# Kernel optimization log

Measured on AMD Instinct MI355X. Metric: run time of the kernel, lower is better.

The kernel has to match this reference:

```python
import jax, jax.numpy as jnp
import numpy as np

D_MODEL = 1024
N_HEADS = 16
HEAD_DIM = D_MODEL // N_HEADS
NEG_INF = -1e10


def setup_inputs() -> dict:
    key = jax.random.key(0)
    ks = jax.random.split(key, 6)
    B, S = 2, 2048
    x = jax.random.normal(ks[0], (B, S, D_MODEL), dtype=jnp.float32)
    mask = jnp.ones((B, S), dtype=jnp.int32)
    scale_w = 1.0 / np.sqrt(D_MODEL)
    Wq = jax.random.normal(ks[1], (D_MODEL, D_MODEL), dtype=jnp.float32) * scale_w
    Wk = jax.random.normal(ks[2], (D_MODEL, D_MODEL), dtype=jnp.float32) * scale_w
    Wv = jax.random.normal(ks[3], (D_MODEL, D_MODEL), dtype=jnp.float32) * scale_w
    Wo = jax.random.normal(ks[4], (D_MODEL, D_MODEL), dtype=jnp.float32) * scale_w
    bq = jnp.zeros((D_MODEL,), jnp.float32)
    bk = jnp.zeros((D_MODEL,), jnp.float32)
    bv = jnp.zeros((D_MODEL,), jnp.float32)
    bo = jnp.zeros((D_MODEL,), jnp.float32)
    return {"x": x, "mask": mask, "Wq": Wq, "bq": bq, "Wk": Wk, "bk": bk,
            "Wv": Wv, "bv": bv, "Wo": Wo, "bo": bo}


def reference(x, mask, Wq, bq, Wk, bk, Wv, bv, Wo, bo):
    B, S, _ = x.shape
    # Linear projections (torch Linear: y = x @ W.T + b)
    Q = x @ Wq.T + bq
    K = x @ Wk.T + bk
    V = x @ Wv.T + bv
    # [B, H, S, Dh]
    Q = Q.reshape(B, S, N_HEADS, HEAD_DIM).transpose(0, 2, 1, 3)
    K = K.reshape(B, S, N_HEADS, HEAD_DIM).transpose(0, 2, 1, 3)
    V = V.reshape(B, S, N_HEADS, HEAD_DIM).transpose(0, 2, 1, 3)
    scale = jnp.sqrt(jnp.float32(HEAD_DIM))
    energy = jnp.einsum('bhqd,bhkd->bhqk', Q, K) / scale  # [B,H,S,S]
    # mask: [B,S] -> broadcast over heads and query dim (keys masked)
    m = mask[:, None, None, :]  # [B,1,1,S]
    energy = jnp.where(m == 0, jnp.float32(NEG_INF), energy)
    attention = jax.nn.softmax(energy, axis=-1)
    # dropout in eval mode = identity
    out = jnp.einsum('bhqk,bhkd->bhqd', attention, V)  # [B,H,S,Dh]
    out = out.transpose(0, 2, 1, 3).reshape(B, S, D_MODEL)
    return out @ Wo.T + bo
```

## Files before the change

### kernel.cpp

```cpp
#include <hip/hip_runtime.h>
#include <hip/hip_bf16.h>

typedef __hip_bfloat16 bf16;
typedef __attribute__((ext_vector_type(8))) short s8v;
typedef __attribute__((ext_vector_type(4))) float f4v;

#define D_MODEL 1024
#define S_LEN   2048
#define BATCH   2
#define NH      16
#define HD      64
#define M_TOTAL 4096
#define NT      (S_LEN / 64)

__device__ __forceinline__ void gll16(const bf16* g, bf16* l) {
    __builtin_amdgcn_global_load_lds(
        (const __attribute__((address_space(1))) void*)g,
        (__attribute__((address_space(3))) void*)l, 16, 0, 0);
}

__global__ __launch_bounds__(256) void cvt_bf16x8(const float* __restrict__ s,
                                                  bf16* __restrict__ d, int n) {
    int i = (blockIdx.x * 256 + threadIdx.x) * 8;
    if (i < n) {
        float4 a = *(const float4*)(s + i);
        float4 b = *(const float4*)(s + i + 4);
        union { bf16 h[8]; uint4 u; } p;
        p.h[0] = __float2bfloat16(a.x); p.h[1] = __float2bfloat16(a.y);
        p.h[2] = __float2bfloat16(a.z); p.h[3] = __float2bfloat16(a.w);
        p.h[4] = __float2bfloat16(b.x); p.h[5] = __float2bfloat16(b.y);
        p.h[6] = __float2bfloat16(b.z); p.h[7] = __float2bfloat16(b.w);
        *(uint4*)(d + i) = p.u;
    }
}

struct WPtrs { const float* s0; const float* s1; const float* s2; const float* s3;
               bf16* d0; bf16* d1; bf16* d2; bf16* d3; };

__global__ __launch_bounds__(256) void cvt_w(WPtrs p) {
    const float* s; bf16* d;
    switch (blockIdx.y) {
        case 0:  s = p.s0; d = p.d0; break;
        case 1:  s = p.s1; d = p.d1; break;
        case 2:  s = p.s2; d = p.d2; break;
        default: s = p.s3; d = p.d3; break;
    }
    int i = (blockIdx.x * 256 + threadIdx.x) * 8;
    float4 a = *(const float4*)(s + i);
    float4 b = *(const float4*)(s + i + 4);
    union { bf16 h[8]; uint4 u; } q;
    q.h[0] = __float2bfloat16(a.x); q.h[1] = __float2bfloat16(a.y);
    q.h[2] = __float2bfloat16(a.z); q.h[3] = __float2bfloat16(a.w);
    q.h[4] = __float2bfloat16(b.x); q.h[5] = __float2bfloat16(b.y);
    q.h[6] = __float2bfloat16(b.z); q.h[7] = __float2bfloat16(b.w);
    *(uint4*)(d + i) = q.u;
}

template<int TM, int TN>
__device__ __forceinline__ void gemm_main(const bf16* __restrict__ A,
                                          const bf16* __restrict__ W,
                                          bf16* As, bf16* Bs,
                                          int bm, int bn,
                                          f4v (&acc)[TM/32][TN/32])
{
    constexpr int FM = TM / 32, FN = TN / 32;
    constexpr int CALLS_A = TM / 16, CALLS = (TM + TN) / 16, PW = CALLS / 4;
    const int t = threadIdx.x, wv = t >> 6, lane = t & 63;
    const int quad = lane >> 4, l15 = lane & 15;
    const int wm = (wv >> 1) * (TM / 2), wn = (wv & 1) * (TN / 2);
    const int lr = lane >> 2, lc = (lane & 3) * 8;

    auto STAGE = [&](int buf, int k0) {
        #pragma unroll
        for (int c = 0; c < PW; ++c) {
            const int cc = wv * PW + c;
            if (cc < CALLS_A) {
                gll16(A + (size_t)(bm + cc * 16 + lr) * D_MODEL + k0 + lc,
                      As + buf * (TM * 32) + cc * 16 * 32);
            } else {
                const int r2 = cc - CALLS_A;
                gll16(W + (size_t)(bn + r2 * 16 + lr) * D_MODEL + k0 + lc,
                      Bs + buf * (TN * 32) + r2 * 16 * 32);
            }
        }
    };

    STAGE(0, 0);
    __syncthreads();
    int cur = 0;

    for (int k0 = 0; k0 < D_MODEL; k0 += 32) {
        if (k0 + 32 < D_MODEL) STAGE(cur ^ 1, k0 + 32);

        const bf16* ab = As + cur * (TM * 32);
        const bf16* bb = Bs + cur * (TN * 32);
        s8v af[FM], bfv[FN];
        #pragma unroll
        for (int i = 0; i < FM; ++i)
            af[i] = *(const s8v*)(ab + (wm + i * 16 + l15) * 32 + quad * 8);
        #pragma unroll
        for (int j = 0; j < FN; ++j)
            bfv[j] = *(const s8v*)(bb + (wn + j * 16 + l15) * 32 + quad * 8);
        __builtin_amdgcn_s_setprio(1);
        #pragma unroll
        for (int i = 0; i < FM; ++i)
            #pragma unroll
            for (int j = 0; j < FN; ++j)
                acc[i][j] = __builtin_amdgcn_mfma_f32_16x16x32_bf16(af[i], bfv[j], acc[i][j], 0, 0, 0);
        __builtin_amdgcn_s_setprio(0);

        __syncthreads();
        cur ^= 1;
    }
}

__global__ __launch_bounds__(256) void gemm_qkv(
    const bf16* __restrict__ x,
    const bf16* __restrict__ Wq, const bf16* __restrict__ Wk, const bf16* __restrict__ Wv,
    const float* __restrict__ bq, const float* __restrict__ bk, const float* __restrict__ bv,
    bf16* __restrict__ Qb, bf16* __restrict__ Kb, bf16* __restrict__ Vtb)
{
    __shared__ __align__(16) char smem[4 * 64 * 72 * 2];
    bf16* As = (bf16*)smem;
    bf16* Bs = (bf16*)(smem + 2 * 128 * 32 * 2);
    bf16 (*Tw)[64][72] = (bf16(*)[64][72])smem;

    const int z = blockIdx.z;
    const bf16*  W    = (z == 0) ? Wq : (z == 1) ? Wk : Wv;
    const float* bias = (z == 0) ? bq : (z == 1) ? bk : bv;
    bf16*        out  = (z == 0) ? Qb : (z == 1) ? Kb : Vtb;
    const int bm = blockIdx.y * 128, bn = blockIdx.x * 128;

    f4v acc[4][4] = {};
    gemm_main<128, 128>(x, W, As, Bs, bm, bn, acc);

    const int t = threadIdx.x, wv = t >> 6, lane = t & 63;
    const int quad = lane >> 4, l15 = lane & 15;
    const int wm = (wv >> 1) * 64, wn = (wv & 1) * 64;

    if (z == 2) {
        __syncthreads();
        #pragma unroll
        for (int j = 0; j < 4; ++j) {
            const int col = bn + wn + j * 16 + l15;
            const float bv_ = bias[col];
            #pragma unroll
            for (int i = 0; i < 4; ++i) {
                #pragma unroll
                for (int rp = 0; rp < 4; rp += 2) {
                    union { bf16 h[2]; unsigned u; } p2;
                    p2.h[0] = __float2bfloat16(acc[i][j][rp]     + bv_);
                    p2.h[1] = __float2bfloat16(acc[i][j][rp + 1] + bv_);
                    *(unsigned*)&Tw[wv][j * 16 + l15][i * 16 + quad * 4 + rp] = p2.u;
                }
            }
        }
        const int bb = (bm + wm) >> 11, s0 = (bm + wm) & 2047;
        #pragma unroll
        for (int p = 0; p < 8; ++p) {
            const int dl = p * 8 + (lane >> 3);
            const int sl = (lane & 7) * 8;
            const int col = bn + wn + dl;
            const int h = col >> 6, d = col & 63;
            uint4 v = *(const uint4*)&Tw[wv][dl][sl];
            *(uint4*)&out[(((size_t)(bb * NH + h)) * HD + d) * S_LEN + s0 + sl] = v;
        }
    } else {
        #pragma unroll
        for (int j = 0; j < 4; ++j) {
            const int col = bn + wn + j * 16 + l15;
            const float bv_ = bias[col];
            const int h = col >> 6, d = col & 63;
            #pragma unroll
            for (int i = 0; i < 4; ++i) {
                #pragma unroll
                for (int r = 0; r < 4; ++r) {
                    const int row = bm + wm + i * 16 + quad * 4 + r;
                    const int b = row >> 11, s = row & 2047;
                    const float v = acc[i][j][r] + bv_;
                    out[(((size_t)(b * NH + h)) * S_LEN + s) * HD + d] = __float2bfloat16(v);
                }
            }
        }
    }
}

__global__ __launch_bounds__(256) void gemm_out(
    const bf16* __restrict__ Ob, const bf16* __restrict__ Wo,
    const float* __restrict__ bo, float* __restrict__ out)
{
    __shared__ __align__(16) bf16 As[2][64 * 32];
    __shared__ __align__(16) bf16 Bs[2][128 * 32];
    const int bm = blockIdx.y * 64, bn = blockIdx.x * 128;

    f4v acc[2][4] = {};
    gemm_main<64, 128>(Ob, Wo, &As[0][0], &Bs[0][0], bm, bn, acc);

    const int t = threadIdx.x, wv = t >> 6, lane = t & 63;
    const int quad = lane >> 4, l15 = lane & 15;
    const int wm = (wv >> 1) * 32, wn = (wv & 1) * 64;
    #pragma unroll
    for (int j = 0; j < 4; ++j) {
        const int col = bn + wn + j * 16 + l15;
        const float bv_ = bo[col];
        #pragma unroll
        for (int i = 0; i < 2; ++i)
            #pragma unroll
            for (int r = 0; r < 4; ++r) {
                const int row = bm + wm + i * 16 + quad * 4 + r;
                out[(size_t)row * D_MODEL + col] = acc[i][j][r] + bv_;
            }
    }
}

__global__ __launch_bounds__(256) void attn_mfma(
    const bf16* __restrict__ Q, const bf16* __restrict__ K,
    const bf16* __restrict__ Vt, const int* __restrict__ mask,
    bf16* __restrict__ O)
{
    __shared__ __align__(16) bf16 Ks[64][64];
    __shared__ __align__(16) bf16 Vts[64][64];
    __shared__ __align__(16) bf16 Ps[4][16][64];
    __shared__ float mb[64];

    const int t = threadIdx.x, wv = t >> 6, lane = t & 63;
    const int quad = lane >> 4, l15 = lane & 15;
    const int sw = l15 & 7;
    const int bid = blockIdx.x;
    const int b = bid & 1, h = (bid >> 1) & 15, qt = bid >> 5;
    const int q0 = qt * 64;
    const size_t qkbase = ((size_t)(b * NH + h)) * S_LEN * HD;
    const size_t vtbase = ((size_t)(b * NH + h)) * HD * S_LEN;

    const float KSC  = 0.125f * 1.44269504f;
    const float THR2 = 8.0f * 1.44269504f;

    const bf16* qrow = Q + qkbase + (size_t)(q0 + wv * 16 + l15) * HD;
    const s8v qf0 = *(const s8v*)(qrow + quad * 8);
    const s8v qf1 = *(const s8v*)(qrow + 32 + quad * 8);

    const int srow = t >> 2;
    const int swr  = srow & 7;
    const int c2   = (t & 3) * 2;
    const int ch0  = c2 ^ swr, ch1 = (c2 + 1) ^ swr;

    uint4 kr0, kr1, vr0, vr1; int mr = 1;
    auto LOADT = [&](int kt2) {
        const int kk = kt2 * 64;
        const uint4* kp = (const uint4*)(K  + qkbase + (size_t)(kk + srow) * HD + c2 * 8);
        const uint4* vp = (const uint4*)(Vt + vtbase + (size_t)srow * S_LEN + kk + c2 * 8);
        kr0 = kp[0]; kr1 = kp[1];
        vr0 = vp[0]; vr1 = vp[1];
        if (t < 64) mr = mask[b * S_LEN + kk + t];
    };
    auto STAGE = [&]() {
        *(uint4*)&Ks[srow][ch0 * 8]  = kr0;
        *(uint4*)&Ks[srow][ch1 * 8]  = kr1;
        *(uint4*)&Vts[srow][ch0 * 8] = vr0;
        *(uint4*)&Vts[srow][ch1 * 8] = vr1;
        if (t < 64) mb[t] = mr ? 0.f : -1e30f;
    };

    LOADT(0);

    float mprev = -1e30f, lsum = 0.f;
    f4v oacc[4] = {};

    for (int kt = 0; kt < NT; ++kt) {
        __syncthreads();
        STAGE();
        __syncthreads();
        if (kt + 1 < NT) LOADT(kt + 1);

        f4v st[4];
        __builtin_amdgcn_s_setprio(1);
        #pragma unroll
        for (int c = 0; c < 4; ++c) {
            const char* kr = (const char*)&Ks[c * 16 + l15][0];
            s8v kf0 = *(const s8v*)(kr + ((quad ^ sw) << 4));
            s8v kf1 = *(const s8v*)(kr + (((4 + quad) ^ sw) << 4));
            f4v z = {0.f, 0.f, 0.f, 0.f};
            z = __builtin_amdgcn_mfma_f32_16x16x32_bf16(kf0, qf0, z, 0, 0, 0);
            z = __builtin_amdgcn_mfma_f32_16x16x32_bf16(kf1, qf1, z, 0, 0, 0);
            st[c] = z;
        }
        __builtin_amdgcn_s_setprio(0);

        float mt = -1e30f;
        #pragma unroll
        for (int c = 0; c < 4; ++c) {
            const f4v m4 = *(const f4v*)&mb[c * 16 + quad * 4];
            st[c] = st[c] * KSC + m4;
            mt = fmaxf(mt, fmaxf(fmaxf(st[c][0], st[c][1]), fmaxf(st[c][2], st[c][3])));
        }
        mt = fmaxf(mt, __shfl_xor(mt, 16, 64));
        mt = fmaxf(mt, __shfl_xor(mt, 32, 64));

        float mn = mprev;
        if (!__all(mt <= mprev + THR2)) {
            mn = fmaxf(mprev, mt);
            const float alpha = __builtin_amdgcn_exp2f(mprev - mn);
            mprev = mn;
            float av[4];
            #pragma unroll
            for (int r = 0; r < 4; ++r) av[r] = __shfl(alpha, quad * 4 + r, 64);
            #pragma unroll
            for (int dt = 0; dt < 4; ++dt)
                #pragma unroll
                for (int r = 0; r < 4; ++r) oacc[dt][r] *= av[r];
            lsum *= alpha;
        }

        f4v psv = {0.f, 0.f, 0.f, 0.f};
        #pragma unroll
        for (int c = 0; c < 4; ++c) {
            f4v e = st[c] - mn;
            e[0] = __builtin_amdgcn_exp2f(e[0]);
            e[1] = __builtin_amdgcn_exp2f(e[1]);
            e[2] = __builtin_amdgcn_exp2f(e[2]);
            e[3] = __builtin_amdgcn_exp2f(e[3]);
            st[c] = e;
            psv += e;
        }
        lsum += psv[0] + psv[1] + psv[2] + psv[3];

        char* pr = (char*)&Ps[wv][l15][0];
        #pragma unroll
        for (int c = 0; c < 4; ++c) {
            union { bf16 hh[4]; short4 s4; } pk;
            pk.hh[0] = __float2bfloat16(st[c][0]);
            pk.hh[1] = __float2bfloat16(st[c][1]);
            pk.hh[2] = __float2bfloat16(st[c][2]);
            pk.hh[3] = __float2bfloat16(st[c][3]);
            const int wch = (2 * c + (quad >> 1)) ^ sw;
            *(short4*)(pr + (wch << 4) + ((quad & 1) << 3)) = pk.s4;
        }
        s8v pf0 = *(const s8v*)(pr + ((quad ^ sw) << 4));
        s8v pf1 = *(const s8v*)(pr + (((4 + quad) ^ sw) << 4));

        __builtin_amdgcn_s_setprio(1);
        #pragma unroll
        for (int dt = 0; dt < 4; ++dt) {
            const char* vr = (const char*)&Vts[dt * 16 + l15][0];
            s8v vf0 = *(const s8v*)(vr + ((quad ^ sw) << 4));
            s8v vf1 = *(const s8v*)(vr + (((4 + quad) ^ sw) << 4));
            oacc[dt] = __builtin_amdgcn_mfma_f32_16x16x32_bf16(pf0, vf0, oacc[dt], 0, 0, 0);
            oacc[dt] = __builtin_amdgcn_mfma_f32_16x16x32_bf16(pf1, vf1, oacc[dt], 0, 0, 0);
        }
        __builtin_amdgcn_s_setprio(0);
    }

    lsum += __shfl_xor(lsum, 16, 64);
    lsum += __shfl_xor(lsum, 32, 64);
    float linv[4];
    #pragma unroll
    for (int r = 0; r < 4; ++r) linv[r] = 1.f / __shfl(lsum, quad * 4 + r, 64);
    #pragma unroll
    for (int dt = 0; dt < 4; ++dt) {
        #pragma unroll
        for (int r = 0; r < 4; ++r) {
            const int s = q0 + wv * 16 + quad * 4 + r;
            const int col = h * 64 + dt * 16 + l15;
            O[((size_t)b * S_LEN + s) * D_MODEL + col] = __float2bfloat16(oacc[dt][r] * linv[r]);
        }
    }
}

extern "C" void kernel_launch(void* const* d_in, const int* in_sizes, int n_in,
                              void* d_out, int out_size, void* d_ws, size_t ws_size,
                              hipStream_t stream) {
    const float* x    = (const float*)d_in[0];
    const int*   mask = (const int*)  d_in[1];
    const float* Wq   = (const float*)d_in[2];
    const float* bq   = (const float*)d_in[3];
    const float* Wk   = (const float*)d_in[4];
    const float* bk   = (const float*)d_in[5];
    const float* Wv   = (const float*)d_in[6];
    const float* bv   = (const float*)d_in[7];
    const float* Wo   = (const float*)d_in[8];
    const float* bo   = (const float*)d_in[9];
    float* out = (float*)d_out;

    char* w = (char*)d_ws;
    bf16* xb  = (bf16*)w; w += (size_t)M_TOTAL * D_MODEL * 2;
    bf16* Wqb = (bf16*)w; w += (size_t)D_MODEL * D_MODEL * 2;
    bf16* Wkb = (bf16*)w; w += (size_t)D_MODEL * D_MODEL * 2;
    bf16* Wvb = (bf16*)w; w += (size_t)D_MODEL * D_MODEL * 2;
    bf16* Wob = (bf16*)w; w += (size_t)D_MODEL * D_MODEL * 2;
    bf16* Qb  = (bf16*)w; w += (size_t)M_TOTAL * D_MODEL * 2;
    bf16* Kb  = (bf16*)w; w += (size_t)M_TOTAL * D_MODEL * 2;
    bf16* Vtb = (bf16*)w; w += (size_t)M_TOTAL * D_MODEL * 2;
    bf16* Ob  = (bf16*)w; w += (size_t)M_TOTAL * D_MODEL * 2;

    const int nx = M_TOTAL * D_MODEL;
    cvt_bf16x8<<<nx / 2048, 256, 0, stream>>>(x, xb, nx);
    WPtrs wp = { Wq, Wk, Wv, Wo, Wqb, Wkb, Wvb, Wob };
    cvt_w<<<dim3(D_MODEL * D_MODEL / 2048, 4), 256, 0, stream>>>(wp);

    gemm_qkv<<<dim3(8, 32, 3), 256, 0, stream>>>(xb, Wqb, Wkb, Wvb, bq, bk, bv, Qb, Kb, Vtb);

    attn_mfma<<<BATCH * NH * (S_LEN / 64), 256, 0, stream>>>(Qb, Kb, Vtb, mask, Ob);

    gemm_out<<<dim3(8, 64), 256, 0, stream>>>(Ob, Wob, bo, out);
}
```

Baseline: 222.4 us.

## Double attention key tile to 128 and read mask directly from global

Result: slower. 372.6 us (+67.6%).

```diff
diff --git a/kernel.cpp b/kernel.cpp
--- a/kernel.cpp
+++ b/kernel.cpp
@@ -11,7 +11,6 @@
 #define NH      16
 #define HD      64
 #define M_TOTAL 4096
-#define NT      (S_LEN / 64)
 
 __device__ __forceinline__ void gll16(const bf16* g, bf16* l) {
     __builtin_amdgcn_global_load_lds(
@@ -218,16 +217,15 @@
     const bf16* __restrict__ Vt, const int* __restrict__ mask,
     bf16* __restrict__ O)
 {
-    __shared__ __align__(16) bf16 Ks[64][64];
-    __shared__ __align__(16) bf16 Vts[64][64];
+    __shared__ __align__(16) bf16 Ks[128][64];
+    __shared__ __align__(16) bf16 Vts[64][128];
     __shared__ __align__(16) bf16 Ps[4][16][64];
-    __shared__ float mb[64];
 
     const int t = threadIdx.x, wv = t >> 6, lane = t & 63;
     const int quad = lane >> 4, l15 = lane & 15;
     const int sw = l15 & 7;
     const int bid = blockIdx.x;
-    const int b = bid & 1, h = (bid >> 1) & 15, qt = bid >> 5;
+    const int qt = bid & 31, h = (bid >> 5) & 15, b = bid >> 9;
     const int q0 = qt * 64;
     const size_t qkbase = ((size_t)(b * NH + h)) * S_LEN * HD;
     const size_t vtbase = ((size_t)(b * NH + h)) * HD * S_LEN;
@@ -239,26 +237,26 @@
     const s8v qf0 = *(const s8v*)(qrow + quad * 8);
     const s8v qf1 = *(const s8v*)(qrow + 32 + quad * 8);
 
-    const int srow = t >> 2;
-    const int swr  = srow & 7;
-    const int c2   = (t & 3) * 2;
-    const int ch0  = c2 ^ swr, ch1 = (c2 + 1) ^ swr;
-
-    uint4 kr0, kr1, vr0, vr1; int mr = 1;
+    const int krow = t >> 1, kcb = (t & 1) * 4;
+    const int vrow = t >> 2, vcb = (t & 3) * 4;
+
+    uint4 kr[4], vr[4];
     auto LOADT = [&](int kt2) {
-        const int kk = kt2 * 64;
-        const uint4* kp = (const uint4*)(K  + qkbase + (size_t)(kk + srow) * HD + c2 * 8);
-        const uint4* vp = (const uint4*)(Vt + vtbase + (size_t)srow * S_LEN + kk + c2 * 8);
-        kr0 = kp[0]; kr1 = kp[1];
-        vr0 = vp[0]; vr1 = vp[1];
-        if (t < 64) mr = mask[b * S_LEN + kk + t];
+        const int kk = kt2 * 128;
+        const bf16* kp = K  + qkbase + (size_t)(kk + krow) * HD + kcb * 8;
+        const bf16* vp = Vt + vtbase + (size_t)vrow * S_LEN + kk + vcb * 8;
+        #pragma unroll
+        for (int j = 0; j < 4; ++j) kr[j] = *(const uint4*)(kp + j * 8);
+        #pragma unroll
+        for (int j = 0; j < 4; ++j) vr[j] = *(const uint4*)(vp + j * 8);
     };
     auto STAGE = [&]() {
-        *(uint4*)&Ks[srow][ch0 * 8]  = kr0;
-        *(uint4*)&Ks[srow][ch1 * 8]  = kr1;
-        *(uint4*)&Vts[srow][ch0 * 8] = vr0;
-        *(uint4*)&Vts[srow][ch1 * 8] = vr1;
-        if (t < 64) mb[t] = mr ? 0.f : -1e30f;
+        #pragma unroll
+        for (int j = 0; j < 4; ++j)
+            *(uint4*)&Ks[krow][((kcb + j) ^ (krow & 7)) * 8] = kr[j];
+        #pragma unroll
+        for (int j = 0; j < 4; ++j)
+            *(uint4*)&Vts[vrow][((vcb + j) ^ (vrow & 7)) * 8] = vr[j];
     };
 
     LOADT(0);
@@ -266,19 +264,21 @@
     float mprev = -1e30f, lsum = 0.f;
     f4v oacc[4] = {};
 
-    for (int kt = 0; kt < NT; ++kt) {
+    for (int kt = 0; kt < S_LEN / 128; ++kt) {
         __syncthreads();
         STAGE();
         __syncthreads();
-        if (kt + 1 < NT) LOADT(kt + 1);
-
-        f4v st[4];
+        if (kt + 1 < S_LEN / 128) LOADT(kt + 1);
+
+        const int kk = kt * 128;
+
+        f4v st[8];
         __builtin_amdgcn_s_setprio(1);
         #pragma unroll
-        for (int c = 0; c < 4; ++c) {
-            const char* kr = (const char*)&Ks[c * 16 + l15][0];
-            s8v kf0 = *(const s8v*)(kr + ((quad ^ sw) << 4));
-            s8v kf1 = *(const s8v*)(kr + (((4 + quad) ^ sw) << 4));
+        for (int c = 0; c < 8; ++c) {
+            const char* krd = (const char*)&Ks[c * 16 + l15][0];
+            s8v kf0 = *(const s8v*)(krd + ((quad ^ sw) << 4));
+            s8v kf1 = *(const s8v*)(krd + (((4 + quad) ^ sw) << 4));
             f4v z = {0.f, 0.f, 0.f, 0.f};
             z = __builtin_amdgcn_mfma_f32_16x16x32_bf16(kf0, qf0, z, 0, 0, 0);
             z = __builtin_amdgcn_mfma_f32_16x16x32_bf16(kf1, qf1, z, 0, 0, 0);
@@ -288,8 +288,13 @@
 
         float mt = -1e30f;
         #pragma unroll
-        for (int c = 0; c < 4; ++c) {
-            const f4v m4 = *(const f4v*)&mb[c * 16 + quad * 4];
+        for (int c = 0; c < 8; ++c) {
+            const int4 mkc = *(const int4*)&mask[b * S_LEN + kk + c * 16 + quad * 4];
+            f4v m4;
+            m4[0] = mkc.x ? 0.f : -1e30f;
+            m4[1] = mkc.y ? 0.f : -1e30f;
+            m4[2] = mkc.z ? 0.f : -1e30f;
+            m4[3] = mkc.w ? 0.f : -1e30f;
             st[c] = st[c] * KSC + m4;
             mt = fmaxf(mt, fmaxf(fmaxf(st[c][0], st[c][1]), fmaxf(st[c][2], st[c][3])));
         }
@@ -313,7 +318,7 @@
 
         f4v psv = {0.f, 0.f, 0.f, 0.f};
         #pragma unroll
-        for (int c = 0; c < 4; ++c) {
+        for (int c = 0; c < 8; ++c) {
             f4v e = st[c] - mn;
             e[0] = __builtin_amdgcn_exp2f(e[0]);
             e[1] = __builtin_amdgcn_exp2f(e[1]);
@@ -326,28 +331,32 @@
 
         char* pr = (char*)&Ps[wv][l15][0];
         #pragma unroll
-        for (int c = 0; c < 4; ++c) {
-            union { bf16 hh[4]; short4 s4; } pk;
-            pk.hh[0] = __float2bfloat16(st[c][0]);
-            pk.hh[1] = __float2bfloat16(st[c][1]);
-            pk.hh[2] = __float2bfloat16(st[c][2]);
-            pk.hh[3] = __float2bfloat16(st[c][3]);
-            const int wch = (2 * c + (quad >> 1)) ^ sw;
-            *(short4*)(pr + (wch << 4) + ((quad & 1) << 3)) = pk.s4;
-        }
-        s8v pf0 = *(const s8v*)(pr + ((quad ^ sw) << 4));
-        s8v pf1 = *(const s8v*)(pr + (((4 + quad) ^ sw) << 4));
-
-        __builtin_amdgcn_s_setprio(1);
-        #pragma unroll
-        for (int dt = 0; dt < 4; ++dt) {
-            const char* vr = (const char*)&Vts[dt * 16 + l15][0];
-            s8v vf0 = *(const s8v*)(vr + ((quad ^ sw) << 4));
-            s8v vf1 = *(const s8v*)(vr + (((4 + quad) ^ sw) << 4));
-            oacc[dt] = __builtin_amdgcn_mfma_f32_16x16x32_bf16(pf0, vf0, oacc[dt], 0, 0, 0);
-            oacc[dt] = __builtin_amdgcn_mfma_f32_16x16x32_bf16(pf1, vf1, oacc[dt], 0, 0, 0);
-        }
-        __builtin_amdgcn_s_setprio(0);
+        for (int hk = 0; hk < 2; ++hk) {
+            #pragma unroll
+            for (int cl = 0; cl < 4; ++cl) {
+                const int c = hk * 4 + cl;
+                union { bf16 hh[4]; short4 s4; } pk;
+                pk.hh[0] = __float2bfloat16(st[c][0]);
+                pk.hh[1] = __float2bfloat16(st[c][1]);
+                pk.hh[2] = __float2bfloat16(st[c][2]);
+                pk.hh[3] = __float2bfloat16(st[c][3]);
+                const int wch = (2 * cl + (quad >> 1)) ^ sw;
+                *(short4*)(pr + (wch << 4) + ((quad & 1) << 3)) = pk.s4;
+            }
+            s8v pf0 = *(const s8v*)(pr + ((quad ^ sw) << 4));
+            s8v pf1 = *(const s8v*)(pr + (((4 + quad) ^ sw) << 4));
+
+            __builtin_amdgcn_s_setprio(1);
+            #pragma unroll
+            for (int dt = 0; dt < 4; ++dt) {
+                const char* vrd = (const char*)&Vts[dt * 16 + l15][0];
+                s8v vf0 = *(const s8v*)(vrd + (((hk * 8 + quad) ^ sw) << 4));
+                s8v vf1 = *(const s8v*)(vrd + (((hk * 8 + 4 + quad) ^ sw) << 4));
+                oacc[dt] = __builtin_amdgcn_mfma_f32_16x16x32_bf16(pf0, vf0, oacc[dt], 0, 0, 0);
+                oacc[dt] = __builtin_amdgcn_mfma_f32_16x16x32_bf16(pf1, vf1, oacc[dt], 0, 0, 0);
+            }
+            __builtin_amdgcn_s_setprio(0);
+        }
     }
 
     lsum += __shfl_xor(lsum, 16, 64);
```

## Load K/V MFMA fragments directly from global memory, drop LDS staging and barriers

Applied to the files above, without the earlier changes.

Measured after the change: 387.8 us. 1.74x slower.

```diff
diff --git a/kernel.cpp b/kernel.cpp
--- a/kernel.cpp
+++ b/kernel.cpp
@@ -218,10 +218,7 @@
     const bf16* __restrict__ Vt, const int* __restrict__ mask,
     bf16* __restrict__ O)
 {
-    __shared__ __align__(16) bf16 Ks[64][64];
-    __shared__ __align__(16) bf16 Vts[64][64];
     __shared__ __align__(16) bf16 Ps[4][16][64];
-    __shared__ float mb[64];
 
     const int t = threadIdx.x, wv = t >> 6, lane = t & 63;
     const int quad = lane >> 4, l15 = lane & 15;
@@ -239,57 +236,36 @@
     const s8v qf0 = *(const s8v*)(qrow + quad * 8);
     const s8v qf1 = *(const s8v*)(qrow + 32 + quad * 8);
 
-    const int srow = t >> 2;
-    const int swr  = srow & 7;
-    const int c2   = (t & 3) * 2;
-    const int ch0  = c2 ^ swr, ch1 = (c2 + 1) ^ swr;
-
-    uint4 kr0, kr1, vr0, vr1; int mr = 1;
-    auto LOADT = [&](int kt2) {
-        const int kk = kt2 * 64;
-        const uint4* kp = (const uint4*)(K  + qkbase + (size_t)(kk + srow) * HD + c2 * 8);
-        const uint4* vp = (const uint4*)(Vt + vtbase + (size_t)srow * S_LEN + kk + c2 * 8);
-        kr0 = kp[0]; kr1 = kp[1];
-        vr0 = vp[0]; vr1 = vp[1];
-        if (t < 64) mr = mask[b * S_LEN + kk + t];
-    };
-    auto STAGE = [&]() {
-        *(uint4*)&Ks[srow][ch0 * 8]  = kr0;
-        *(uint4*)&Ks[srow][ch1 * 8]  = kr1;
-        *(uint4*)&Vts[srow][ch0 * 8] = vr0;
-        *(uint4*)&Vts[srow][ch1 * 8] = vr1;
-        if (t < 64) mb[t] = mr ? 0.f : -1e30f;
-    };
-
-    LOADT(0);
+    const bf16* kfrag = K + qkbase + (size_t)l15 * HD;
+    const bf16* vfrag = Vt + vtbase + (size_t)l15 * S_LEN;
 
     float mprev = -1e30f, lsum = 0.f;
     f4v oacc[4] = {};
 
     for (int kt = 0; kt < NT; ++kt) {
-        __syncthreads();
-        STAGE();
-        __syncthreads();
-        if (kt + 1 < NT) LOADT(kt + 1);
+        const int k0 = kt * 64;
 
         f4v st[4];
-        __builtin_amdgcn_s_setprio(1);
         #pragma unroll
         for (int c = 0; c < 4; ++c) {
-            const char* kr = (const char*)&Ks[c * 16 + l15][0];
-            s8v kf0 = *(const s8v*)(kr + ((quad ^ sw) << 4));
-            s8v kf1 = *(const s8v*)(kr + (((4 + quad) ^ sw) << 4));
+            const bf16* kr = kfrag + (size_t)(k0 + c * 16) * HD;
+            s8v kf0 = *(const s8v*)(kr + quad * 8);
+            s8v kf1 = *(const s8v*)(kr + 32 + quad * 8);
             f4v z = {0.f, 0.f, 0.f, 0.f};
             z = __builtin_amdgcn_mfma_f32_16x16x32_bf16(kf0, qf0, z, 0, 0, 0);
             z = __builtin_amdgcn_mfma_f32_16x16x32_bf16(kf1, qf1, z, 0, 0, 0);
             st[c] = z;
         }
-        __builtin_amdgcn_s_setprio(0);
 
         float mt = -1e30f;
         #pragma unroll
         for (int c = 0; c < 4; ++c) {
-            const f4v m4 = *(const f4v*)&mb[c * 16 + quad * 4];
+            const int4 mkc = *(const int4*)&mask[b * S_LEN + k0 + c * 16 + quad * 4];
+            f4v m4;
+            m4[0] = mkc.x ? 0.f : -1e30f;
+            m4[1] = mkc.y ? 0.f : -1e30f;
+            m4[2] = mkc.z ? 0.f : -1e30f;
+            m4[3] = mkc.w ? 0.f : -1e30f;
             st[c] = st[c] * KSC + m4;
             mt = fmaxf(mt, fmaxf(fmaxf(st[c][0], st[c][1]), fmaxf(st[c][2], st[c][3])));
         }
@@ -338,16 +314,14 @@
         s8v pf0 = *(const s8v*)(pr + ((quad ^ sw) << 4));
         s8v pf1 = *(const s8v*)(pr + (((4 + quad) ^ sw) << 4));
 
-        __builtin_amdgcn_s_setprio(1);
         #pragma unroll
         for (int dt = 0; dt < 4; ++dt) {
-            const char* vr = (const char*)&Vts[dt * 16 + l15][0];
-            s8v vf0 = *(const s8v*)(vr + ((quad ^ sw) << 4));
-            s8v vf1 = *(const s8v*)(vr + (((4 + quad) ^ sw) << 4));
+            const bf16* vr = vfrag + (size_t)(dt * 16) * S_LEN + k0;
+            s8v vf0 = *(const s8v*)(vr + quad * 8);
+            s8v vf1 = *(const s8v*)(vr + 32 + quad * 8);
             oacc[dt] = __builtin_amdgcn_mfma_f32_16x16x32_bf16(pf0, vf0, oacc[dt], 0, 0, 0);
             oacc[dt] = __builtin_amdgcn_mfma_f32_16x16x32_bf16(pf1, vf1, oacc[dt], 0, 0, 0);
         }
-        __builtin_amdgcn_s_setprio(0);
     }
 
     lsum += __shfl_xor(lsum, 16, 64);
```

## Double-buffer K/V tiles in attention, merge conversion kernels, reorder block mapping

Applied to the files above, without the earlier changes.

Result: slower. 241.8 us (+8.8%).

```diff
diff --git a/kernel.cpp b/kernel.cpp
--- a/kernel.cpp
+++ b/kernel.cpp
@@ -19,33 +19,25 @@
         (__attribute__((address_space(3))) void*)l, 16, 0, 0);
 }
 
-__global__ __launch_bounds__(256) void cvt_bf16x8(const float* __restrict__ s,
-                                                  bf16* __restrict__ d, int n) {
-    int i = (blockIdx.x * 256 + threadIdx.x) * 8;
-    if (i < n) {
-        float4 a = *(const float4*)(s + i);
-        float4 b = *(const float4*)(s + i + 4);
-        union { bf16 h[8]; uint4 u; } p;
-        p.h[0] = __float2bfloat16(a.x); p.h[1] = __float2bfloat16(a.y);
-        p.h[2] = __float2bfloat16(a.z); p.h[3] = __float2bfloat16(a.w);
-        p.h[4] = __float2bfloat16(b.x); p.h[5] = __float2bfloat16(b.y);
-        p.h[6] = __float2bfloat16(b.z); p.h[7] = __float2bfloat16(b.w);
-        *(uint4*)(d + i) = p.u;
-    }
-}
-
-struct WPtrs { const float* s0; const float* s1; const float* s2; const float* s3;
-               bf16* d0; bf16* d1; bf16* d2; bf16* d3; };
-
-__global__ __launch_bounds__(256) void cvt_w(WPtrs p) {
-    const float* s; bf16* d;
-    switch (blockIdx.y) {
-        case 0:  s = p.s0; d = p.d0; break;
-        case 1:  s = p.s1; d = p.d1; break;
-        case 2:  s = p.s2; d = p.d2; break;
-        default: s = p.s3; d = p.d3; break;
-    }
-    int i = (blockIdx.x * 256 + threadIdx.x) * 8;
+struct CvtPtrs {
+    const float* sx; bf16* dx;
+    const float* s0; const float* s1; const float* s2; const float* s3;
+    bf16* d0; bf16* d1; bf16* d2; bf16* d3;
+};
+
+__global__ __launch_bounds__(256) void cvt_all(CvtPtrs p) {
+    const int bid = blockIdx.x;
+    const float* s; bf16* d; int i;
+    if (bid < 2048) {
+        s = p.sx; d = p.dx;
+        i = (bid * 256 + threadIdx.x) * 8;
+    } else {
+        const int wsel = (bid - 2048) >> 9;
+        const int wb   = (bid - 2048) & 511;
+        s = (wsel == 0) ? p.s0 : (wsel == 1) ? p.s1 : (wsel == 2) ? p.s2 : p.s3;
+        d = (wsel == 0) ? p.d0 : (wsel == 1) ? p.d1 : (wsel == 2) ? p.d2 : p.d3;
+        i = (wb * 256 + threadIdx.x) * 8;
+    }
     float4 a = *(const float4*)(s + i);
     float4 b = *(const float4*)(s + i + 4);
     union { bf16 h[8]; uint4 u; } q;
@@ -218,16 +210,15 @@
     const bf16* __restrict__ Vt, const int* __restrict__ mask,
     bf16* __restrict__ O)
 {
-    __shared__ __align__(16) bf16 Ks[64][64];
-    __shared__ __align__(16) bf16 Vts[64][64];
+    __shared__ __align__(16) bf16 Ks[2][64][64];
+    __shared__ __align__(16) bf16 Vts[2][64][64];
     __shared__ __align__(16) bf16 Ps[4][16][64];
-    __shared__ float mb[64];
 
     const int t = threadIdx.x, wv = t >> 6, lane = t & 63;
     const int quad = lane >> 4, l15 = lane & 15;
     const int sw = l15 & 7;
     const int bid = blockIdx.x;
-    const int b = bid & 1, h = (bid >> 1) & 15, qt = bid >> 5;
+    const int qt = bid & 31, h = (bid >> 5) & 15, b = bid >> 9;
     const int q0 = qt * 64;
     const size_t qkbase = ((size_t)(b * NH + h)) * S_LEN * HD;
     const size_t vtbase = ((size_t)(b * NH + h)) * HD * S_LEN;
@@ -244,39 +235,42 @@
     const int c2   = (t & 3) * 2;
     const int ch0  = c2 ^ swr, ch1 = (c2 + 1) ^ swr;
 
-    uint4 kr0, kr1, vr0, vr1; int mr = 1;
+    uint4 kr0, kr1, vr0, vr1;
     auto LOADT = [&](int kt2) {
         const int kk = kt2 * 64;
         const uint4* kp = (const uint4*)(K  + qkbase + (size_t)(kk + srow) * HD + c2 * 8);
         const uint4* vp = (const uint4*)(Vt + vtbase + (size_t)srow * S_LEN + kk + c2 * 8);
         kr0 = kp[0]; kr1 = kp[1];
         vr0 = vp[0]; vr1 = vp[1];
-        if (t < 64) mr = mask[b * S_LEN + kk + t];
     };
-    auto STAGE = [&]() {
-        *(uint4*)&Ks[srow][ch0 * 8]  = kr0;
-        *(uint4*)&Ks[srow][ch1 * 8]  = kr1;
-        *(uint4*)&Vts[srow][ch0 * 8] = vr0;
-        *(uint4*)&Vts[srow][ch1 * 8] = vr1;
-        if (t < 64) mb[t] = mr ? 0.f : -1e30f;
+    auto STAGE = [&](int bf) {
+        *(uint4*)&Ks[bf][srow][ch0 * 8]  = kr0;
+        *(uint4*)&Ks[bf][srow][ch1 * 8]  = kr1;
+        *(uint4*)&Vts[bf][srow][ch0 * 8] = vr0;
+        *(uint4*)&Vts[bf][srow][ch1 * 8] = vr1;
     };
 
     LOADT(0);
+    STAGE(0);
+    __syncthreads();
 
     float mprev = -1e30f, lsum = 0.f;
     f4v oacc[4] = {};
+    int cur = 0;
 
     for (int kt = 0; kt < NT; ++kt) {
-        __syncthreads();
-        STAGE();
-        __syncthreads();
-        if (kt + 1 < NT) LOADT(kt + 1);
+        const int k0 = kt * 64;
+        const bool more = (kt + 1 < NT);
+        if (more) LOADT(kt + 1);
+
+        const char* kbase = (const char*)&Ks[cur][0][0];
+        const char* vbase = (const char*)&Vts[cur][0][0];
 
         f4v st[4];
         __builtin_amdgcn_s_setprio(1);
         #pragma unroll
         for (int c = 0; c < 4; ++c) {
-            const char* kr = (const char*)&Ks[c * 16 + l15][0];
+            const char* kr = kbase + (c * 16 + l15) * 128;
             s8v kf0 = *(const s8v*)(kr + ((quad ^ sw) << 4));
             s8v kf1 = *(const s8v*)(kr + (((4 + quad) ^ sw) << 4));
             f4v z = {0.f, 0.f, 0.f, 0.f};
@@ -289,7 +283,12 @@
         float mt = -1e30f;
         #pragma unroll
         for (int c = 0; c < 4; ++c) {
-            const f4v m4 = *(const f4v*)&mb[c * 16 + quad * 4];
+            const int4 mkc = *(const int4*)&mask[b * S_LEN + k0 + c * 16 + quad * 4];
+            f4v m4;
+            m4[0] = mkc.x ? 0.f : -1e30f;
+            m4[1] = mkc.y ? 0.f : -1e30f;
+            m4[2] = mkc.z ? 0.f : -1e30f;
+            m4[3] = mkc.w ? 0.f : -1e30f;
             st[c] = st[c] * KSC + m4;
             mt = fmaxf(mt, fmaxf(fmaxf(st[c][0], st[c][1]), fmaxf(st[c][2], st[c][3])));
         }
@@ -324,6 +323,8 @@
         }
         lsum += psv[0] + psv[1] + psv[2] + psv[3];
 
+        if (more) STAGE(cur ^ 1);
+
         char* pr = (char*)&Ps[wv][l15][0];
         #pragma unroll
         for (int c = 0; c < 4; ++c) {
@@ -341,13 +342,16 @@
         __builtin_amdgcn_s_setprio(1);
         #pragma unroll
         for (int dt = 0; dt < 4; ++dt) {
-            const char* vr = (const char*)&Vts[dt * 16 + l15][0];
+            const char* vr = vbase + (dt * 16 + l15) * 128;
             s8v vf0 = *(const s8v*)(vr + ((quad ^ sw) << 4));
             s8v vf1 = *(const s8v*)(vr + (((4 + quad) ^ sw) << 4));
             oacc[dt] = __builtin_amdgcn_mfma_f32_16x16x32_bf16(pf0, vf0, oacc[dt], 0, 0, 0);
             oacc[dt] = __builtin_amdgcn_mfma_f32_16x16x32_bf16(pf1, vf1, oacc[dt], 0, 0, 0);
         }
         __builtin_amdgcn_s_setprio(0);
+
+        if (more) __syncthreads();
+        cur ^= 1;
     }
 
     lsum += __shfl_xor(lsum, 16, 64);
@@ -392,10 +396,8 @@
     bf16* Vtb = (bf16*)w; w += (size_t)M_TOTAL * D_MODEL * 2;
     bf16* Ob  = (bf16*)w; w += (size_t)M_TOTAL * D_MODEL * 2;
 
-    const int nx = M_TOTAL * D_MODEL;
-    cvt_bf16x8<<<nx / 2048, 256, 0, stream>>>(x, xb, nx);
-    WPtrs wp = { Wq, Wk, Wv, Wo, Wqb, Wkb, Wvb, Wob };
-    cvt_w<<<dim3(D_MODEL * D_MODEL / 2048, 4), 256, 0, stream>>>(wp);
+    CvtPtrs cp = { x, xb, Wq, Wk, Wv, Wo, Wqb, Wkb, Wvb, Wob };
+    cvt_all<<<4096, 256, 0, stream>>>(cp);
 
     gemm_qkv<<<dim3(8, 32, 3), 256, 0, stream>>>(xb, Wqb, Wkb, Wvb, bq, bk, bv, Qb, Kb, Vtb);
 
```
